# Performance work log

Hardware: AMD Instinct MI355X
Metric: run time of the kernel (lower is better)

The kernel has to match this reference:

```python
import jax, jax.numpy as jnp
import numpy as np

DIM = 768
HEADS = 12


def setup_inputs() -> dict:
    key = jax.random.key(0)
    k1, k2, k3, k4 = jax.random.split(key, 4)
    x = jax.random.normal(k1, (8, 1024, DIM), dtype=jnp.float32)
    # qkv: Linear(dim, 3*dim, bias=False); torch stores weight as (out, in), y = x @ W.T
    w_qkv = jax.random.normal(k2, (3 * DIM, DIM), dtype=jnp.float32) * (DIM ** -0.5)
    w_fc = jax.random.normal(k3, (DIM, DIM), dtype=jnp.float32) * (DIM ** -0.5)
    b_fc = jax.random.normal(k4, (DIM,), dtype=jnp.float32) * 0.02
    return {"x": x, "w_qkv": w_qkv, "w_fc": w_fc, "b_fc": b_fc}


def reference(x, w_qkv, w_fc, b_fc):
    b, n, dim = x.shape
    h = HEADS
    d = dim // h
    qkv = jnp.einsum('bnd,ed->bne', x, w_qkv)  # [b, n, 3*dim]
    q, k, v = jnp.split(qkv, 3, axis=-1)
    # b n (h d) -> b h n d
    q = q.reshape(b, n, h, d).transpose(0, 2, 1, 3)
    k = k.reshape(b, n, h, d).transpose(0, 2, 1, 3)
    v = v.reshape(b, n, h, d).transpose(0, 2, 1, 3)
    # NOTE: original module computes d_k = dim**-0.5 but never applies it.
    scores = jnp.einsum('bhqd,bhkd->bhqk', q, k)  # unscaled, faithful to source
    attn = jax.nn.softmax(scores, axis=-1)
    out = jnp.einsum('bhqk,bhkd->bhqd', attn, v)
    out = out.transpose(0, 2, 1, 3).reshape(b, n, dim)  # b h n d -> b n (h d)
    out = jnp.einsum('bnd,ed->bne', out, w_fc) + b_fc
    return out
```

## Files before the change

### kernel.cpp

```cpp
#include <hip/hip_runtime.h>
#include <cstdint>
#include <cstddef>

typedef __bf16 bf16;
typedef __bf16 bf16x4 __attribute__((ext_vector_type(4)));
typedef __bf16 bf16x8 __attribute__((ext_vector_type(8)));
typedef float f32x4 __attribute__((ext_vector_type(4)));
typedef float f32x16 __attribute__((ext_vector_type(16)));

typedef const __attribute__((address_space(1))) void* gas_ptr;
typedef __attribute__((address_space(3))) void* las_ptr;

#define GLOAD_LDS16(g, l) __builtin_amdgcn_global_load_lds((gas_ptr)(g), (las_ptr)(l), 16, 0, 0)

__global__ void cvt_f32_bf16(const float* __restrict__ in, bf16* __restrict__ out, int n4) {
  int i = blockIdx.x * blockDim.x + threadIdx.x;
  int stride = gridDim.x * blockDim.x;
  for (; i < n4; i += stride) {
    float4 v = reinterpret_cast<const float4*>(in)[i];
    bf16x4 o;
    o[0] = (bf16)v.x; o[1] = (bf16)v.y; o[2] = (bf16)v.z; o[3] = (bf16)v.w;
    reinterpret_cast<bf16x4*>(out)[i] = o;
  }
}

__global__ __launch_bounds__(512, 2) void gemm256(
    const bf16* __restrict__ A, const bf16* __restrict__ B,
    int M, int N, int K, bf16* __restrict__ outb) {
  __shared__ bf16 lds[2][32768];
  const int tid = threadIdx.x;
  const int l = tid & 63;
  const int w = tid >> 6;
  const int wr = w >> 2, wc = w & 3;
  const int lr = l & 15, lg = l >> 4;

  const int bid = blockIdx.y * gridDim.x + blockIdx.x;
  const int xcd = bid & 7, c = bid >> 3;
  const int brow = (xcd * 4 + (c & 3)) * 256;
  const int bcol = (c >> 2) * 256;

  const bf16* asrc[4];
  const bf16* bsrc[4];
  int adst[4], bdst[4];
#pragma unroll
  for (int t = 0; t < 4; t++) {
    const int ai = w * 4 + t, kh = ai >> 4, s = ai & 15;
    asrc[t] = A + (size_t)(brow + s * 16 + lr) * K + kh * 32 + lg * 8;
    bsrc[t] = B + (size_t)(bcol + s * 16 + lr) * K + kh * 32 + lg * 8;
    adst[t] = kh * 8192 + s * 512 + l * 8;
    bdst[t] = 16384 + kh * 8192 + s * 512 + l * 8;
  }

  f32x4 acc[8][4] = {};

#pragma unroll
  for (int t = 0; t < 4; t++) {
    GLOAD_LDS16(asrc[t], &lds[0][adst[t]]);
    GLOAD_LDS16(bsrc[t], &lds[0][bdst[t]]);
  }

  const int NS = K >> 6;
  int p = 0;
  for (int step = 0; step < NS; step++) {
    const int k0 = step << 6;
    const int kn = (step + 1 < NS) ? k0 + 64 : k0;
    asm volatile("s_waitcnt vmcnt(0)" ::: "memory");
    __builtin_amdgcn_sched_barrier(0);
    __builtin_amdgcn_s_barrier();
    __builtin_amdgcn_sched_barrier(0);
    const int q = p ^ 1;
    bf16x8 bfr[4];

    {
      bf16x8 af[4];
#pragma unroll
      for (int j = 0; j < 4; j++)
        bfr[j] = *reinterpret_cast<const bf16x8*>(&lds[p][16384 + (wc * 4 + j) * 512 + l * 8]);
#pragma unroll
      for (int i = 0; i < 4; i++)
        af[i] = *reinterpret_cast<const bf16x8*>(&lds[p][(wr * 8 + i) * 512 + l * 8]);
      GLOAD_LDS16(asrc[0] + kn, &lds[q][adst[0]]);
      GLOAD_LDS16(asrc[1] + kn, &lds[q][adst[1]]);
      GLOAD_LDS16(bsrc[0] + kn, &lds[q][bdst[0]]);
      __builtin_amdgcn_sched_barrier(0);
      __builtin_amdgcn_s_setprio(1);
#pragma unroll
      for (int i = 0; i < 4; i++)
#pragma unroll
        for (int j = 0; j < 4; j++)
          acc[i][j] = __builtin_amdgcn_mfma_f32_16x16x32_bf16(af[i], bfr[j], acc[i][j], 0, 0, 0);
      __builtin_amdgcn_s_setprio(0);
      __builtin_amdgcn_sched_barrier(0);
      __builtin_amdgcn_s_barrier();
    }
    {
      bf16x8 af[4];
#pragma unroll
      for (int i = 0; i < 4; i++)
        af[i] = *reinterpret_cast<const bf16x8*>(&lds[p][(wr * 8 + 4 + i) * 512 + l * 8]);
      GLOAD_LDS16(asrc[2] + kn, &lds[q][adst[2]]);
      GLOAD_LDS16(asrc[3] + kn, &lds[q][adst[3]]);
      GLOAD_LDS16(bsrc[1] + kn, &lds[q][bdst[1]]);
      __builtin_amdgcn_sched_barrier(0);
      __builtin_amdgcn_s_setprio(1);
#pragma unroll
      for (int i = 0; i < 4; i++)
#pragma unroll
        for (int j = 0; j < 4; j++)
          acc[4 + i][j] = __builtin_amdgcn_mfma_f32_16x16x32_bf16(af[i], bfr[j], acc[4 + i][j], 0, 0, 0);
      __builtin_amdgcn_s_setprio(0);
      __builtin_amdgcn_sched_barrier(0);
      __builtin_amdgcn_s_barrier();
    }
    {
      bf16x8 af[4];
#pragma unroll
      for (int j = 0; j < 4; j++)
        bfr[j] = *reinterpret_cast<const bf16x8*>(&lds[p][16384 + 8192 + (wc * 4 + j) * 512 + l * 8]);
#pragma unroll
      for (int i = 0; i < 4; i++)
        af[i] = *reinterpret_cast<const bf16x8*>(&lds[p][8192 + (wr * 8 + i) * 512 + l * 8]);
      GLOAD_LDS16(bsrc[2] + kn, &lds[q][bdst[2]]);
      GLOAD_LDS16(bsrc[3] + kn, &lds[q][bdst[3]]);
      __builtin_amdgcn_sched_barrier(0);
      __builtin_amdgcn_s_setprio(1);
#pragma unroll
      for (int i = 0; i < 4; i++)
#pragma unroll
        for (int j = 0; j < 4; j++)
          acc[i][j] = __builtin_amdgcn_mfma_f32_16x16x32_bf16(af[i], bfr[j], acc[i][j], 0, 0, 0);
      __builtin_amdgcn_s_setprio(0);
      __builtin_amdgcn_sched_barrier(0);
      __builtin_amdgcn_s_barrier();
    }
    {
      bf16x8 af[4];
#pragma unroll
      for (int i = 0; i < 4; i++)
        af[i] = *reinterpret_cast<const bf16x8*>(&lds[p][8192 + (wr * 8 + 4 + i) * 512 + l * 8]);
      __builtin_amdgcn_sched_barrier(0);
      __builtin_amdgcn_s_setprio(1);
#pragma unroll
      for (int i = 0; i < 4; i++)
#pragma unroll
        for (int j = 0; j < 4; j++)
          acc[4 + i][j] = __builtin_amdgcn_mfma_f32_16x16x32_bf16(af[i], bfr[j], acc[4 + i][j], 0, 0, 0);
      __builtin_amdgcn_s_setprio(0);
    }
    p = q;
  }

#pragma unroll
  for (int si = 0; si < 8; si++)
#pragma unroll
    for (int r = 0; r < 4; r++) {
      const int m = brow + (wr * 8 + si) * 16 + lg * 4 + r;
#pragma unroll
      for (int j = 0; j < 4; j++) {
        const int e = bcol + (wc * 4 + j) * 16 + lr;
        outb[(size_t)m * N + e] = (bf16)acc[si][j][r];
      }
    }
}

template <int MODE>
__global__ __launch_bounds__(512, 4) void gemm_bt(
    const bf16* __restrict__ A, const bf16* __restrict__ B,
    int M, int N, int K,
    bf16* __restrict__ outb, float* __restrict__ outf,
    const float* __restrict__ bias) {
  constexpr int BK = 32;
  __shared__ bf16 lds[3][12288];
  const int tid = threadIdx.x;
  const int l = tid & 63;
  const int w = tid >> 6;
  const int wr = w >> 1, wc = w & 1;
  const int lr = l & 15, lg = l >> 4;

  const int bid = blockIdx.y * 32 + blockIdx.x;
  const int xcd = bid & 7, c = bid >> 3;
  const int brow = (xcd * 4 + (c & 3)) * 256;
  const int bcol = (c >> 2) * 128;

  const bf16* sa0 = A + (size_t)(brow + w * 16 + lr) * K + lg * 8;
  const bf16* sa1 = sa0 + (size_t)128 * K;
  const bf16* sb0 = B + (size_t)(bcol + w * 16 + lr) * K + lg * 8;
  const int dA0 = w * 512 + l * 8;
  const int dA1 = (8 + w) * 512 + l * 8;
  const int dB0 = 8192 + w * 512 + l * 8;

  f32x4 acc[4][4] = {};

  GLOAD_LDS16(sa0, &lds[0][dA0]);
  GLOAD_LDS16(sa1, &lds[0][dA1]);
  GLOAD_LDS16(sb0, &lds[0][dB0]);
  GLOAD_LDS16(sa0 + BK, &lds[1][dA0]);
  GLOAD_LDS16(sa1 + BK, &lds[1][dA1]);
  GLOAD_LDS16(sb0 + BK, &lds[1][dB0]);

  int p = 0;
  for (int k0 = 0; k0 < K; k0 += BK) {
    asm volatile("s_waitcnt vmcnt(3)" ::: "memory");
    __builtin_amdgcn_sched_barrier(0);
    __builtin_amdgcn_s_barrier();
    __builtin_amdgcn_sched_barrier(0);

    int kn = k0 + 2 * BK;
    if (kn >= K) kn = k0;
    const int pt = (p >= 1) ? p - 1 : 2;
    GLOAD_LDS16(sa0 + kn, &lds[pt][dA0]);
    GLOAD_LDS16(sa1 + kn, &lds[pt][dA1]);
    GLOAD_LDS16(sb0 + kn, &lds[pt][dB0]);

    bf16x8 af[4], bfr[4];
#pragma unroll
    for (int mi = 0; mi < 4; mi++)
      af[mi] = *reinterpret_cast<const bf16x8*>(&lds[p][(wr * 4 + mi) * 512 + l * 8]);
#pragma unroll
    for (int ni = 0; ni < 4; ni++)
      bfr[ni] = *reinterpret_cast<const bf16x8*>(&lds[p][8192 + (wc * 4 + ni) * 512 + l * 8]);
#pragma unroll
    for (int mi = 0; mi < 4; mi++)
#pragma unroll
      for (int ni = 0; ni < 4; ni++)
        acc[mi][ni] = __builtin_amdgcn_mfma_f32_16x16x32_bf16(af[mi], bfr[ni], acc[mi][ni], 0, 0, 0);
    p = (p == 2) ? 0 : p + 1;
  }

#pragma unroll
  for (int mi = 0; mi < 4; mi++) {
#pragma unroll
    for (int r = 0; r < 4; r++) {
      const int m = brow + wr * 64 + mi * 16 + lg * 4 + r;
#pragma unroll
      for (int ni = 0; ni < 4; ni++) {
        const int e = bcol + wc * 64 + ni * 16 + lr;
        const float v = acc[mi][ni][r];
        if (MODE == 1) {
          outf[(size_t)m * N + e] = v + bias[e];
        } else {
          outb[(size_t)m * N + e] = (bf16)v;
        }
      }
    }
  }
}

__global__ __launch_bounds__(256) void vtrans(const bf16* __restrict__ qkv,
                                              bf16* __restrict__ vtb) {
  __shared__ bf16 t[64 * 72];
  const int bh = blockIdx.x;
  const int b = bh / 12, h = bh % 12;
  const int nt = blockIdx.y;
  const int tid = threadIdx.x;
#pragma unroll
  for (int it = 0; it < 2; it++) {
    const int item = tid + it * 256;
    const int nl = item >> 3, c = item & 7;
    bf16x8 v = *reinterpret_cast<const bf16x8*>(
        &qkv[(size_t)(b * 1024 + nt * 64 + nl) * 2304 + 1536 + h * 64 + c * 8]);
#pragma unroll
    for (int j = 0; j < 8; j++) t[(c * 8 + j) * 72 + nl] = v[j];
  }
  __syncthreads();
#pragma unroll
  for (int it = 0; it < 2; it++) {
    const int item = tid + it * 256;
    const int d = item >> 3, c2 = item & 7;
    bf16x8 v = *reinterpret_cast<const bf16x8*>(&t[d * 72 + c2 * 8]);
    *reinterpret_cast<bf16x8*>(
        &vtb[(size_t)bh * 65536 + d * 1024 + nt * 64 + c2 * 8]) = v;
  }
}

__global__ __launch_bounds__(256, 3) void attn_kernel(
    const bf16* __restrict__ QKV, const bf16* __restrict__ Vt,
    bf16* __restrict__ Out) {
  __shared__ bf16 Kb[2][4096];
  __shared__ bf16 Vb[2][4096];
  const int tid = threadIdx.x;
  const int l = tid & 63;
  const int w = tid >> 6;
  const int ql = l & 31;
  const int hi = l >> 5;
  const int bh = blockIdx.x;
  const int b = bh / 12, h = bh % 12;
  const int q0 = blockIdx.y * 128 + w * 32;
  const bf16* Vh = Vt + (size_t)bh * 65536;
  constexpr float L2E = 1.4426950408889634f;

  const int kdst0 = (0 * 4 + w) * 512 + l * 8;
  const int kdst1 = (1 * 4 + w) * 512 + l * 8;
  const bf16* ksrc0 = QKV + (size_t)(b * 1024 + ql) * 2304 + 768 + h * 64 + w * 16 + hi * 8;
  const bf16* ksrc1 = ksrc0 + (size_t)32 * 2304;
  const bf16* vsrc0 = Vh + (size_t)((w & 1) * 32 + ql) * 1024 + ((0 * 4 + w) >> 1) * 16 + hi * 8;
  const bf16* vsrc1 = Vh + (size_t)((w & 1) * 32 + ql) * 1024 + ((1 * 4 + w) >> 1) * 16 + hi * 8;

  const bf16* Qrow = QKV + (size_t)(b * 1024 + q0 + ql) * 2304 + h * 64;
  bf16x8 qf[4];
#pragma unroll
  for (int s = 0; s < 4; s++)
    qf[s] = *reinterpret_cast<const bf16x8*>(&Qrow[s * 16 + hi * 8]);

  f32x16 o[2] = {};
  float ls0 = 0.f, ls1 = 0.f, ls2 = 0.f, ls3 = 0.f;

  GLOAD_LDS16(ksrc0, &Kb[0][kdst0]);
  GLOAD_LDS16(ksrc1, &Kb[0][kdst1]);
  GLOAD_LDS16(vsrc0, &Vb[0][kdst0]);
  GLOAD_LDS16(vsrc1, &Vb[0][kdst1]);
  asm volatile("s_waitcnt vmcnt(0)" ::: "memory");
  __syncthreads();

  int p = 0;
  for (int it = 0; it < 16; ++it) {
    const int kt = it * 64;
    if (it < 15) {
      GLOAD_LDS16(ksrc0 + (size_t)(kt + 64) * 2304, &Kb[p ^ 1][kdst0]);
      GLOAD_LDS16(ksrc1 + (size_t)(kt + 64) * 2304, &Kb[p ^ 1][kdst1]);
      GLOAD_LDS16(vsrc0 + (kt + 64), &Vb[p ^ 1][kdst0]);
      GLOAD_LDS16(vsrc1 + (kt + 64), &Vb[p ^ 1][kdst1]);
    }

    bf16x8 kf[8];
#pragma unroll
    for (int r = 0; r < 8; r++)
      kf[r] = *reinterpret_cast<const bf16x8*>(&Kb[p][r * 512 + l * 8]);
    f32x16 st0 = {}, st1 = {};
    __builtin_amdgcn_s_setprio(1);
#pragma unroll
    for (int s = 0; s < 4; s++) {
      st0 = __builtin_amdgcn_mfma_f32_32x32x16_bf16(kf[s], qf[s], st0, 0, 0, 0);
      st1 = __builtin_amdgcn_mfma_f32_32x32x16_bf16(kf[4 + s], qf[s], st1, 0, 0, 0);
    }
    __builtin_amdgcn_s_setprio(0);

#pragma unroll
    for (int r = 0; r < 16; r++) {
      float a0 = st0[r] * L2E, a1 = st1[r] * L2E;
      float e0, e1;
      asm("v_exp_f32 %0, %1" : "=v"(e0) : "v"(a0));
      asm("v_exp_f32 %0, %1" : "=v"(e1) : "v"(a1));
      st0[r] = e0; st1[r] = e1;
    }
#pragma unroll
    for (int r = 0; r < 16; r += 2) {
      ls0 += st0[r]; ls1 += st0[r + 1];
      ls2 += st1[r]; ls3 += st1[r + 1];
    }

    bf16x8 pfv[4];
#pragma unroll
    for (int t = 0; t < 4; t++) {
      const int c8 = (t & 1) * 8;
      const f32x16& sv = (t < 2) ? st0 : st1;
      uint32_t wA0, wA1, wB0, wB1;
      asm("v_cvt_pk_bf16_f32 %0, %1, %2" : "=v"(wA0) : "v"(sv[c8 + 0]), "v"(sv[c8 + 1]));
      asm("v_cvt_pk_bf16_f32 %0, %1, %2" : "=v"(wA1) : "v"(sv[c8 + 2]), "v"(sv[c8 + 3]));
      asm("v_cvt_pk_bf16_f32 %0, %1, %2" : "=v"(wB0) : "v"(sv[c8 + 4]), "v"(sv[c8 + 5]));
      asm("v_cvt_pk_bf16_f32 %0, %1, %2" : "=v"(wB1) : "v"(sv[c8 + 6]), "v"(sv[c8 + 7]));
      asm("v_permlane32_swap_b32 %0, %1" : "+v"(wA0), "+v"(wB0));
      asm("v_permlane32_swap_b32 %0, %1" : "+v"(wA1), "+v"(wB1));
      union { uint32_t u[4]; bf16x8 v; } pf;
      pf.u[0] = wA0; pf.u[1] = wA1; pf.u[2] = wB0; pf.u[3] = wB1;
      pfv[t] = pf.v;
    }

    bf16x8 vf[8];
#pragma unroll
    for (int r = 0; r < 8; r++)
      vf[r] = *reinterpret_cast<const bf16x8*>(&Vb[p][r * 512 + l * 8]);
    __builtin_amdgcn_s_setprio(1);
#pragma unroll
    for (int t = 0; t < 4; t++) {
      o[0] = __builtin_amdgcn_mfma_f32_32x32x16_bf16(vf[t * 2 + 0], pfv[t], o[0], 0, 0, 0);
      o[1] = __builtin_amdgcn_mfma_f32_32x32x16_bf16(vf[t * 2 + 1], pfv[t], o[1], 0, 0, 0);
    }
    __builtin_amdgcn_s_setprio(0);

    asm volatile("s_waitcnt vmcnt(0)" ::: "memory");
    __syncthreads();
    p ^= 1;
  }

  float lsum = (ls0 + ls1) + (ls2 + ls3);
  lsum += __shfl_xor(lsum, 32);
  const float rl = 1.0f / lsum;
  bf16* orow = Out + (size_t)(b * 1024 + q0 + ql) * 768 + h * 64;
#pragma unroll
  for (int dh = 0; dh < 2; dh++)
#pragma unroll
    for (int rq = 0; rq < 4; rq++) {
      union { ushort us[4]; uint2 v; } pk;
#pragma unroll
      for (int i = 0; i < 4; i++) {
        const bf16 hv = (bf16)(o[dh][rq * 4 + i] * rl);
        pk.us[i] = __builtin_bit_cast(ushort, hv);
      }
      *reinterpret_cast<uint2*>(&orow[dh * 32 + rq * 8 + hi * 4]) = pk.v;
    }
}

extern "C" void kernel_launch(void* const* d_in, const int* in_sizes, int n_in,
                              void* d_out, int out_size, void* d_ws, size_t ws_size,
                              hipStream_t stream) {
  const float* x = (const float*)d_in[0];
  const float* w_qkv = (const float*)d_in[1];
  const float* w_fc = (const float*)d_in[2];
  const float* b_fc = (const float*)d_in[3];
  float* out = (float*)d_out;
  char* ws = (char*)d_ws;

  bf16* xb = (bf16*)(ws);
  bf16* vtb = (bf16*)(ws);
  bf16* wqkb = (bf16*)(ws + 12582912);
  bf16* wfcb = (bf16*)(ws + 16121856);
  bf16* qkvb = (bf16*)(ws + 17301504);
  bf16* aob = (bf16*)(ws + 55050240);

  cvt_f32_bf16<<<2048, 256, 0, stream>>>(x, xb, 6291456 / 4);
  cvt_f32_bf16<<<1728, 256, 0, stream>>>(w_qkv, wqkb, 1769472 / 4);
  cvt_f32_bf16<<<576, 256, 0, stream>>>(w_fc, wfcb, 589824 / 4);

  gemm256<<<dim3(32, 9), 512, 0, stream>>>(xb, wqkb, 8192, 2304, 768, qkvb);

  vtrans<<<dim3(96, 16), 256, 0, stream>>>(qkvb, vtb);

  attn_kernel<<<dim3(96, 8), 256, 0, stream>>>(qkvb, vtb, aob);

  gemm_bt<1><<<dim3(32, 6), 512, 0, stream>>>(aob, wfcb, 8192, 768, 768,
                                              nullptr, out, b_fc);
}
```

Measured before the change: 150.9 us.

## Split gemm256 prefetch by K-half and relax waits to partial vmcnt

Each 64-wide K step of the gemm256 main loop now loads data for the next step in two K-halves. Each wave issues 4 global-to-LDS loads per half. The loop waits with vmcnt(4) instead of vmcnt(0), so the second half's loads stay in flight while the first half is computed. Workgroup barriers drop from four per step to two. This aims to hide global memory latency and cut synchronization stalls, but it relies on the in-order vmcnt accounting being exactly right to avoid LDS read/write races.

```diff
diff --git a/kernel.cpp b/kernel.cpp
--- a/kernel.cpp
+++ b/kernel.cpp
@@ -39,116 +39,102 @@
   const int brow = (xcd * 4 + (c & 3)) * 256;
   const int bcol = (c >> 2) * 256;
 
-  const bf16* asrc[4];
-  const bf16* bsrc[4];
-  int adst[4], bdst[4];
-#pragma unroll
-  for (int t = 0; t < 4; t++) {
-    const int ai = w * 4 + t, kh = ai >> 4, s = ai & 15;
-    asrc[t] = A + (size_t)(brow + s * 16 + lr) * K + kh * 32 + lg * 8;
-    bsrc[t] = B + (size_t)(bcol + s * 16 + lr) * K + kh * 32 + lg * 8;
-    adst[t] = kh * 8192 + s * 512 + l * 8;
-    bdst[t] = 16384 + kh * 8192 + s * 512 + l * 8;
-  }
+  const int s0 = w * 2, s1 = w * 2 + 1;
+  const bf16* aS0 = A + (size_t)(brow + s0 * 16 + lr) * K + lg * 8;
+  const bf16* aS1 = A + (size_t)(brow + s1 * 16 + lr) * K + lg * 8;
+  const bf16* bS0 = B + (size_t)(bcol + s0 * 16 + lr) * K + lg * 8;
+  const bf16* bS1 = B + (size_t)(bcol + s1 * 16 + lr) * K + lg * 8;
+  const int dA0 = s0 * 512 + l * 8, dA1 = s1 * 512 + l * 8;
+  const int dB0 = 16384 + dA0, dB1 = 16384 + dA1;
 
   f32x4 acc[8][4] = {};
 
-#pragma unroll
-  for (int t = 0; t < 4; t++) {
-    GLOAD_LDS16(asrc[t], &lds[0][adst[t]]);
-    GLOAD_LDS16(bsrc[t], &lds[0][bdst[t]]);
-  }
+  GLOAD_LDS16(aS0, &lds[0][dA0]);
+  GLOAD_LDS16(aS1, &lds[0][dA1]);
+  GLOAD_LDS16(bS0, &lds[0][dB0]);
+  GLOAD_LDS16(bS1, &lds[0][dB1]);
+  GLOAD_LDS16(aS0 + 32, &lds[0][dA0 + 8192]);
+  GLOAD_LDS16(aS1 + 32, &lds[0][dA1 + 8192]);
+  GLOAD_LDS16(bS0 + 32, &lds[0][dB0 + 8192]);
+  GLOAD_LDS16(bS1 + 32, &lds[0][dB1 + 8192]);
 
   const int NS = K >> 6;
   int p = 0;
   for (int step = 0; step < NS; step++) {
     const int k0 = step << 6;
     const int kn = (step + 1 < NS) ? k0 + 64 : k0;
-    asm volatile("s_waitcnt vmcnt(0)" ::: "memory");
+    const int q = p ^ 1;
+    bf16x8 bfr[4], af[4];
+
+    asm volatile("s_waitcnt vmcnt(4)" ::: "memory");
     __builtin_amdgcn_sched_barrier(0);
     __builtin_amdgcn_s_barrier();
     __builtin_amdgcn_sched_barrier(0);
-    const int q = p ^ 1;
-    bf16x8 bfr[4];
-
-    {
-      bf16x8 af[4];
+#pragma unroll
+    for (int j = 0; j < 4; j++)
+      bfr[j] = *reinterpret_cast<const bf16x8*>(&lds[p][16384 + (wc * 4 + j) * 512 + l * 8]);
+#pragma unroll
+    for (int i = 0; i < 4; i++)
+      af[i] = *reinterpret_cast<const bf16x8*>(&lds[p][(wr * 8 + i) * 512 + l * 8]);
+    GLOAD_LDS16(aS0 + kn, &lds[q][dA0]);
+    GLOAD_LDS16(aS1 + kn, &lds[q][dA1]);
+    GLOAD_LDS16(bS0 + kn, &lds[q][dB0]);
+    GLOAD_LDS16(bS1 + kn, &lds[q][dB1]);
+    __builtin_amdgcn_sched_barrier(0);
+    __builtin_amdgcn_s_setprio(1);
+#pragma unroll
+    for (int i = 0; i < 4; i++)
 #pragma unroll
       for (int j = 0; j < 4; j++)
-        bfr[j] = *reinterpret_cast<const bf16x8*>(&lds[p][16384 + (wc * 4 + j) * 512 + l * 8]);
-#pragma unroll
-      for (int i = 0; i < 4; i++)
-        af[i] = *reinterpret_cast<const bf16x8*>(&lds[p][(wr * 8 + i) * 512 + l * 8]);
-      GLOAD_LDS16(asrc[0] + kn, &lds[q][adst[0]]);
-      GLOAD_LDS16(asrc[1] + kn, &lds[q][adst[1]]);
-      GLOAD_LDS16(bsrc[0] + kn, &lds[q][bdst[0]]);
-      __builtin_amdgcn_sched_barrier(0);
-      __builtin_amdgcn_s_setprio(1);
-#pragma unroll
-      for (int i = 0; i < 4; i++)
-#pragma unroll
-        for (int j = 0; j < 4; j++)
-          acc[i][j] = __builtin_amdgcn_mfma_f32_16x16x32_bf16(af[i], bfr[j], acc[i][j], 0, 0, 0);
-      __builtin_amdgcn_s_setprio(0);
-      __builtin_amdgcn_sched_barrier(0);
-      __builtin_amdgcn_s_barrier();
-    }
-    {
-      bf16x8 af[4];
-#pragma unroll
-      for (int i = 0; i < 4; i++)
-        af[i] = *reinterpret_cast<const bf16x8*>(&lds[p][(wr * 8 + 4 + i) * 512 + l * 8]);
-      GLOAD_LDS16(asrc[2] + kn, &lds[q][adst[2]]);
-      GLOAD_LDS16(asrc[3] + kn, &lds[q][adst[3]]);
-      GLOAD_LDS16(bsrc[1] + kn, &lds[q][bdst[1]]);
-      __builtin_amdgcn_sched_barrier(0);
-      __builtin_amdgcn_s_setprio(1);
-#pragma unroll
-      for (int i = 0; i < 4; i++)
-#pragma unroll
-        for (int j = 0; j < 4; j++)
-          acc[4 + i][j] = __builtin_amdgcn_mfma_f32_16x16x32_bf16(af[i], bfr[j], acc[4 + i][j], 0, 0, 0);
-      __builtin_amdgcn_s_setprio(0);
-      __builtin_amdgcn_sched_barrier(0);
-      __builtin_amdgcn_s_barrier();
-    }
-    {
-      bf16x8 af[4];
+        acc[i][j] = __builtin_amdgcn_mfma_f32_16x16x32_bf16(af[i], bfr[j], acc[i][j], 0, 0, 0);
+    __builtin_amdgcn_s_setprio(0);
+#pragma unroll
+    for (int i = 0; i < 4; i++)
+      af[i] = *reinterpret_cast<const bf16x8*>(&lds[p][(wr * 8 + 4 + i) * 512 + l * 8]);
+    __builtin_amdgcn_s_setprio(1);
+#pragma unroll
+    for (int i = 0; i < 4; i++)
 #pragma unroll
       for (int j = 0; j < 4; j++)
-        bfr[j] = *reinterpret_cast<const bf16x8*>(&lds[p][16384 + 8192 + (wc * 4 + j) * 512 + l * 8]);
-#pragma unroll
-      for (int i = 0; i < 4; i++)
-        af[i] = *reinterpret_cast<const bf16x8*>(&lds[p][8192 + (wr * 8 + i) * 512 + l * 8]);
-      GLOAD_LDS16(bsrc[2] + kn, &lds[q][bdst[2]]);
-      GLOAD_LDS16(bsrc[3] + kn, &lds[q][bdst[3]]);
-      __builtin_amdgcn_sched_barrier(0);
-      __builtin_amdgcn_s_setprio(1);
-#pragma unroll
-      for (int i = 0; i < 4; i++)
-#pragma unroll
-        for (int j = 0; j < 4; j++)
-          acc[i][j] = __builtin_amdgcn_mfma_f32_16x16x32_bf16(af[i], bfr[j], acc[i][j], 0, 0, 0);
-      __builtin_amdgcn_s_setprio(0);
-      __builtin_amdgcn_sched_barrier(0);
-      __builtin_amdgcn_s_barrier();
-    }
-    {
-      bf16x8 af[4];
-#pragma unroll
-      for (int i = 0; i < 4; i++)
-        af[i] = *reinterpret_cast<const bf16x8*>(&lds[p][8192 + (wr * 8 + 4 + i) * 512 + l * 8]);
-      __builtin_amdgcn_sched_barrier(0);
-      __builtin_amdgcn_s_setprio(1);
-#pragma unroll
-      for (int i = 0; i < 4; i++)
-#pragma unroll
-        for (int j = 0; j < 4; j++)
-          acc[4 + i][j] = __builtin_amdgcn_mfma_f32_16x16x32_bf16(af[i], bfr[j], acc[4 + i][j], 0, 0, 0);
-      __builtin_amdgcn_s_setprio(0);
-    }
+        acc[4 + i][j] = __builtin_amdgcn_mfma_f32_16x16x32_bf16(af[i], bfr[j], acc[4 + i][j], 0, 0, 0);
+    __builtin_amdgcn_s_setprio(0);
+
+    asm volatile("s_waitcnt vmcnt(4)" ::: "memory");
+    __builtin_amdgcn_sched_barrier(0);
+    __builtin_amdgcn_s_barrier();
+    __builtin_amdgcn_sched_barrier(0);
+#pragma unroll
+    for (int j = 0; j < 4; j++)
+      bfr[j] = *reinterpret_cast<const bf16x8*>(&lds[p][16384 + 8192 + (wc * 4 + j) * 512 + l * 8]);
+#pragma unroll
+    for (int i = 0; i < 4; i++)
+      af[i] = *reinterpret_cast<const bf16x8*>(&lds[p][8192 + (wr * 8 + i) * 512 + l * 8]);
+    GLOAD_LDS16(aS0 + kn + 32, &lds[q][dA0 + 8192]);
+    GLOAD_LDS16(aS1 + kn + 32, &lds[q][dA1 + 8192]);
+    GLOAD_LDS16(bS0 + kn + 32, &lds[q][dB0 + 8192]);
+    GLOAD_LDS16(bS1 + kn + 32, &lds[q][dB1 + 8192]);
+    __builtin_amdgcn_sched_barrier(0);
+    __builtin_amdgcn_s_setprio(1);
+#pragma unroll
+    for (int i = 0; i < 4; i++)
+#pragma unroll
+      for (int j = 0; j < 4; j++)
+        acc[i][j] = __builtin_amdgcn_mfma_f32_16x16x32_bf16(af[i], bfr[j], acc[i][j], 0, 0, 0);
+    __builtin_amdgcn_s_setprio(0);
+#pragma unroll
+    for (int i = 0; i < 4; i++)
+      af[i] = *reinterpret_cast<const bf16x8*>(&lds[p][8192 + (wr * 8 + 4 + i) * 512 + l * 8]);
+    __builtin_amdgcn_s_setprio(1);
+#pragma unroll
+    for (int i = 0; i < 4; i++)
+#pragma unroll
+      for (int j = 0; j < 4; j++)
+        acc[4 + i][j] = __builtin_amdgcn_mfma_f32_16x16x32_bf16(af[i], bfr[j], acc[4 + i][j], 0, 0, 0);
+    __builtin_amdgcn_s_setprio(0);
+
     p = q;
   }
+  asm volatile("s_waitcnt vmcnt(0)" ::: "memory");
 
 #pragma unroll
   for (int si = 0; si < 8; si++)
```

Result: faster. 144.1 us (-4.5%).
